# Kernel tuning notes

Measured on AMD Instinct MI355X. Metric: run time of the kernel, lower is better.

## Reference

```python
import jax, jax.numpy as jnp
import numpy as np

CTX_SIZE = 4096
LAYER = 1
N_EMBD = 1024
HEAD_SIZE = 64
B, T = 4, 4096


def setup_inputs() -> dict:
    key = jax.random.key(0)
    ks = jax.random.split(key, 4)
    s = 1.0 / np.sqrt(N_EMBD)
    return {
        "x": jax.random.normal(ks[0], (B, T, N_EMBD), dtype=jnp.float32),
        "Wq": jax.random.normal(ks[1], (N_EMBD, HEAD_SIZE), dtype=jnp.float32) * s,
        "bq": jnp.zeros((HEAD_SIZE,), dtype=jnp.float32),
        "Wk": jax.random.normal(ks[2], (N_EMBD, HEAD_SIZE), dtype=jnp.float32) * s,
        "bk": jnp.zeros((HEAD_SIZE,), dtype=jnp.float32),
        "Wv": jax.random.normal(ks[3], (N_EMBD, HEAD_SIZE), dtype=jnp.float32) * s,
        "bv": jnp.zeros((HEAD_SIZE,), dtype=jnp.float32),
    }


def reference(x, Wq, bq, Wk, bk, Wv, bv):
    Bx, Tx, C = x.shape
    t = CTX_SIZE // (2 ** LAYER)
    cut = min(Tx, t)  # static: shapes are concrete under jit

    k = x @ Wk + bk                      # [B, T, H]
    q = x[:, -cut:, :] @ Wq + bq         # [B, cut, H] (fade: queries on last cut tokens)
    v = x @ Wv + bv                      # [B, T, H]

    att = jnp.einsum("bqh,bkh->bqk", q, k) * (C ** -0.5)  # [B, cut, T]

    # row i corresponds to absolute query position (T - cut + i); causal: key j <= that pos
    q_pos = jnp.arange(cut) + (Tx - cut)   # [cut]
    k_pos = jnp.arange(Tx)                 # [T]
    mask = k_pos[None, :] <= q_pos[:, None]  # [cut, T], True = keep
    att = jnp.where(mask[None, :, :], att, -jnp.inf)
    att = jax.nn.softmax(att, axis=-1)
    # dropout p=0.0 (eval mode): identity

    out = jnp.einsum("bqk,bkh->bqh", att, v)  # [B, cut, H]
    return out
```

## Files before the change

kernel.cpp:

```cpp
#include <hip/hip_runtime.h>

#define BB 4
#define TT 4096
#define CUT 2048
#define CE 1024
#define HD 64
#define QSC 0.045084220027780106f

typedef unsigned short u16;
typedef unsigned int u32;
typedef __attribute__((ext_vector_type(8))) short bf16x8;
typedef __attribute__((ext_vector_type(4))) float f32x4;

__device__ __forceinline__ u16 f2b(float f) {
  union { float f; unsigned u; } v; v.f = f;
  unsigned r = v.u + 0x7fffu + ((v.u >> 16) & 1u);
  return (u16)(r >> 16);
}

__device__ __forceinline__ u32 cvtpk(float lo, float hi) {
  u32 r;
  asm("v_cvt_pk_bf16_f32 %0, %1, %2" : "=v"(r) : "v"(lo), "v"(hi));
  return r;
}

__device__ __forceinline__ void gld16(const u16* g, u16* l) {
  __builtin_amdgcn_global_load_lds((const __attribute__((address_space(1))) u32*)g,
                                   (__attribute__((address_space(3))) u32*)l, 16, 0, 0);
}

__global__ void wtrans_k(const float* __restrict__ Wk, const float* __restrict__ Wv,
                         const float* __restrict__ Wq, u16* __restrict__ w3f) {
  int id = blockIdx.x * 256 + threadIdx.x;
  int j    = id & 7;
  int lane = (id >> 3) & 63;
  int f    = id >> 9;
  int kstep = f & 31;
  int mnt   = f >> 5;
  int m  = mnt >> 2;
  int nt = mnt & 3;
  int k   = kstep * 32 + (lane >> 4) * 8 + j;
  int col = nt * 16 + (lane & 15);
  const float* W = (m == 0) ? Wk : (m == 1) ? Wv : Wq;
  w3f[id] = f2b(W[k * 64 + col]);
}

__launch_bounds__(256, 2)
__global__ void proj_k(const float* __restrict__ x, const u16* __restrict__ w3f,
                       const float* __restrict__ bk, const float* __restrict__ bv,
                       const float* __restrict__ bq,
                       u16* __restrict__ KF, u16* __restrict__ VF, u16* __restrict__ Qb) {
  __shared__ u16  st[2][2][12][512];
  __shared__ f32x4 cl[2][12][64];
  const int tid  = threadIdx.x;
  const int lane = tid & 63;
  const int wv   = tid >> 6;
  const int rg   = wv & 1;
  const int kh   = wv >> 1;
  const int l15  = lane & 15;
  const int g    = lane >> 4;
  const int r0   = blockIdx.x * 32;

  f32x4 acc[12];
  #pragma unroll
  for (int t = 0; t < 12; ++t) acc[t] = (f32x4){0.f, 0.f, 0.f, 0.f};

  const float* xrow = x + (size_t)(r0 + rg * 16 + l15) * CE + kh * 512;

  #define STAGE(buf, t)                                                        \
    {                                                                          \
      _Pragma("unroll")                                                        \
      for (int i = 0; i < 6; ++i) {                                            \
        int jj = wv * 6 + i;                                                   \
        int hh = jj / 12, mm = jj % 12;                                        \
        gld16(&w3f[(size_t)(mm * 32 + hh * 16 + (t)) * 512 + lane * 8],        \
              &st[buf][hh][mm][0]);                                            \
      }                                                                        \
    }

  f32x4 xs[2][2];
  STAGE(0, 0);
  __builtin_amdgcn_sched_barrier(0);
  xs[0][0] = *(const f32x4*)(xrow + g * 8);
  xs[0][1] = *(const f32x4*)(xrow + g * 8 + 4);
  asm volatile("s_waitcnt vmcnt(0)" ::: "memory");
  __builtin_amdgcn_s_barrier();

  #pragma unroll
  for (int t = 0; t < 16; ++t) {
    const int cur = t & 1, nxt = cur ^ 1;
    if (t < 15) {
      STAGE(nxt, t + 1);
      __builtin_amdgcn_sched_barrier(0);
      const float* xp = xrow + (t + 1) * 32 + g * 8;
      xs[nxt][0] = *(const f32x4*)xp;
      xs[nxt][1] = *(const f32x4*)(xp + 4);
      __builtin_amdgcn_sched_barrier(0);
    }
    bf16x8 a;
    #pragma unroll
    for (int j = 0; j < 4; ++j) {
      a[j]     = (short)f2b(xs[cur][0][j]);
      a[j + 4] = (short)f2b(xs[cur][1][j]);
    }
    #pragma unroll
    for (int mnt = 0; mnt < 12; ++mnt) {
      bf16x8 bfr = *(const bf16x8*)&st[cur][kh][mnt][lane * 8];
      acc[mnt] = __builtin_amdgcn_mfma_f32_16x16x32_bf16(a, bfr, acc[mnt], 0, 0, 0);
    }
    if (t < 15) {
      asm volatile("s_waitcnt vmcnt(2)" ::: "memory");
    } else {
      asm volatile("s_waitcnt vmcnt(0)" ::: "memory");
    }
    __builtin_amdgcn_s_barrier();
  }
  #undef STAGE

  if (kh == 1) {
    #pragma unroll
    for (int t = 0; t < 12; ++t) cl[rg][t][lane] = acc[t];
  }
  __syncthreads();
  if (kh == 0) {
    #pragma unroll
    for (int t = 0; t < 12; ++t) acc[t] += cl[rg][t][lane];

    const int b    = r0 >> 12;
    const int cch  = (r0 >> 6) & 63;
    const int half = (r0 >> 5) & 1;
    const int h    = rg;

    const int t0 = r0 & (TT - 1);
    if (t0 >= CUT) {
      const int trow = t0 - CUT + h * 16;
      #pragma unroll
      for (int nt = 0; nt < 4; ++nt) {
        int col = nt * 16 + l15;
        float bc = bq[col];
        #pragma unroll
        for (int r = 0; r < 4; ++r)
          Qb[((size_t)b * CUT + trow + g * 4 + r) * HD + col] =
              f2b((acc[8 + nt][r] + bc) * QSC);
      }
    }
    {
      u16* KFc = KF + ((size_t)(b * 64 + cch) * 8) * 512;
      const int kt2 = (half * 2 + h) * 2;
      #pragma unroll
      for (int nt = 0; nt < 4; ++nt) {
        int col = nt * 16 + l15;
        float bc = bk[col];
        f32x4 v = acc[nt];
        const int off = (kt2 + (nt >> 1)) * 512 + 128 * ((nt & 1) * 2 + (l15 >> 3)) + (l15 & 7);
        #pragma unroll
        for (int r = 0; r < 4; ++r)
          KFc[off + (g * 4 + r) * 8] = f2b(v[r] + bc);
      }
    }
    {
      u16* VFc = VF + ((size_t)(b * 64 + cch) * 8) * 512;
      #pragma unroll
      for (int nt = 0; nt < 4; ++nt) {
        int col = nt * 16 + l15;
        float bc = bv[col];
        f32x4 v = acc[4 + nt];
        #pragma unroll
        for (int r = 0; r < 4; ++r) {
          int tt = h * 16 + g * 4 + r;
          VFc[(half * 4 + nt) * 512 + (l15 + 16 * (tt >> 3)) * 8 + (tt & 7)] = f2b(v[r] + bc);
        }
      }
    }
  }
}

__launch_bounds__(512, 2)
__global__ void attn_k(const u16* __restrict__ Qb, const u16* __restrict__ KF,
                       const u16* __restrict__ VF, float* __restrict__ out) {
  __shared__ u32   PLd[8][16][36];
  __shared__ float OO[8][16][66];
  __shared__ float OL[8][32];
  const int tid  = threadIdx.x;
  const int lane = tid & 63;
  const int wv   = tid >> 6;
  const int l15  = lane & 15;
  const int g    = lane >> 4;
  const int id   = blockIdx.x;
  const int b    = id & 3;
  const int i0   = (id >> 2) * 32;

  const int qmin = CUT + i0;

  bf16x8 qf[2][2];
  #pragma unroll
  for (int h = 0; h < 2; ++h) {
    const u16* qrow = Qb + ((size_t)b * CUT + i0 + h * 16 + l15) * HD;
    qf[h][0] = *(const bf16x8*)&qrow[g * 8];
    qf[h][1] = *(const bf16x8*)&qrow[32 + g * 8];
  }

  f32x4 o[2][4];
  #pragma unroll
  for (int h = 0; h < 2; ++h)
    #pragma unroll
    for (int dt = 0; dt < 4; ++dt) o[h][dt] = (f32x4){0.f, 0.f, 0.f, 0.f};
  float lsum[2] = {0.f, 0.f};

  const int nch = (CUT + i0 + 32 + 63) >> 6;
  const u16* KFb = KF + (size_t)b * 64 * 8 * 512;
  const u16* VFb = VF + (size_t)b * 64 * 8 * 512;

  bf16x8 ka[4][2];
  {
    const u16* kp = KFb + (size_t)wv * 4096 + lane * 8;
    #pragma unroll
    for (int kt = 0; kt < 4; ++kt) {
      ka[kt][0] = *(const bf16x8*)(kp + (kt * 2 + 0) * 512);
      ka[kt][1] = *(const bf16x8*)(kp + (kt * 2 + 1) * 512);
    }
  }

  for (int c = wv; c < nch; c += 8) {
    const int kv0 = c << 6;

    const u16* vp = VFb + (size_t)c * 4096 + lane * 8;
    bf16x8 va[2][4];
    #pragma unroll
    for (int c2 = 0; c2 < 2; ++c2)
      #pragma unroll
      for (int dt = 0; dt < 4; ++dt)
        va[c2][dt] = *(const bf16x8*)(vp + (c2 * 4 + dt) * 512);

    bf16x8 kb[4][2];
    const int cn = c + 8;
    if (cn < nch) {
      const u16* kp = KFb + (size_t)cn * 4096 + lane * 8;
      #pragma unroll
      for (int kt = 0; kt < 4; ++kt) {
        kb[kt][0] = *(const bf16x8*)(kp + (kt * 2 + 0) * 512);
        kb[kt][1] = *(const bf16x8*)(kp + (kt * 2 + 1) * 512);
      }
    }

    f32x4 st[2][4];
    __builtin_amdgcn_s_setprio(1);
    #pragma unroll
    for (int h = 0; h < 2; ++h)
      #pragma unroll
      for (int kt = 0; kt < 4; ++kt) {
        f32x4 s = (f32x4){0.f, 0.f, 0.f, 0.f};
        s = __builtin_amdgcn_mfma_f32_16x16x32_bf16(ka[kt][0], qf[h][0], s, 0, 0, 0);
        s = __builtin_amdgcn_mfma_f32_16x16x32_bf16(ka[kt][1], qf[h][1], s, 0, 0, 0);
        st[h][kt] = s;
      }
    __builtin_amdgcn_s_setprio(0);

    #pragma unroll
    for (int h = 0; h < 2; ++h) {
      if (kv0 + 63 <= qmin + h * 16) {
        #pragma unroll
        for (int kt = 0; kt < 4; ++kt)
          #pragma unroll
          for (int r = 0; r < 4; ++r) {
            float p = exp2f(st[h][kt][r]);
            st[h][kt][r] = p;
            lsum[h] += p;
          }
      } else {
        const int qabs = qmin + h * 16 + l15;
        #pragma unroll
        for (int kt = 0; kt < 4; ++kt)
          #pragma unroll
          for (int r = 0; r < 4; ++r) {
            int key = kv0 + kt * 16 + g * 4 + r;
            float p = exp2f(st[h][kt][r]);
            p = (key <= qabs) ? p : 0.f;
            st[h][kt][r] = p;
            lsum[h] += p;
          }
      }
    }

    #pragma unroll
    for (int h = 0; h < 2; ++h) {
      #pragma unroll
      for (int kt = 0; kt < 4; ++kt) {
        u32 d0 = cvtpk(st[h][kt][0], st[h][kt][1]);
        u32 d1 = cvtpk(st[h][kt][2], st[h][kt][3]);
        u32* p = &PLd[wv][l15][kt * 8 + g * 2];
        p[0] = d0; p[1] = d1;
      }
      __builtin_amdgcn_s_setprio(1);
      #pragma unroll
      for (int c2 = 0; c2 < 2; ++c2) {
        bf16x8 pa = *(const bf16x8*)&PLd[wv][l15][c2 * 16 + g * 4];
        #pragma unroll
        for (int dt = 0; dt < 4; ++dt)
          o[h][dt] = __builtin_amdgcn_mfma_f32_16x16x32_bf16(pa, va[c2][dt], o[h][dt], 0, 0, 0);
      }
      __builtin_amdgcn_s_setprio(0);
    }

    if (cn < nch) {
      #pragma unroll
      for (int kt = 0; kt < 4; ++kt) {
        ka[kt][0] = kb[kt][0];
        ka[kt][1] = kb[kt][1];
      }
    }
  }

  #pragma unroll
  for (int h = 0; h < 2; ++h) {
    float ls = lsum[h];
    ls += __shfl_xor(ls, 16);
    ls += __shfl_xor(ls, 32);
    if (lane < 16) OL[wv][h * 16 + l15] = ls;
  }

  #pragma unroll
  for (int ph = 0; ph < 2; ++ph) {
    #pragma unroll
    for (int dt = 0; dt < 4; ++dt)
      #pragma unroll
      for (int r = 0; r < 4; ++r)
        OO[wv][g * 4 + r][dt * 16 + l15] = o[ph][dt][r];
    __syncthreads();
    #pragma unroll
    for (int e = tid; e < 1024; e += 512) {
      int q = e >> 6, d = e & 63;
      float L = 0.f, O = 0.f;
      #pragma unroll
      for (int w = 0; w < 8; ++w) { L += OL[w][ph * 16 + q]; O += OO[w][q][d]; }
      out[((size_t)b * CUT + i0 + ph * 16 + q) * HD + d] = O / L;
    }
    __syncthreads();
  }
}

extern "C" void kernel_launch(void* const* d_in, const int* in_sizes, int n_in,
                              void* d_out, int out_size, void* d_ws, size_t ws_size,
                              hipStream_t stream) {
  const float* x  = (const float*)d_in[0];
  const float* Wq = (const float*)d_in[1];
  const float* bq = (const float*)d_in[2];
  const float* Wk = (const float*)d_in[3];
  const float* bk = (const float*)d_in[4];
  const float* Wv = (const float*)d_in[5];
  const float* bv = (const float*)d_in[6];
  float* out = (float*)d_out;

  u16* Qb  = (u16*)d_ws;
  u16* W3F = Qb + (size_t)BB * CUT * HD;
  u16* KF  = W3F + (size_t)384 * 512;
  u16* VF  = KF + (size_t)BB * 64 * 8 * 512;

  wtrans_k<<<768, 256, 0, stream>>>(Wk, Wv, Wq, W3F);
  proj_k<<<512, 256, 0, stream>>>(x, W3F, bk, bv, bq, KF, VF, Qb);
  attn_k<<<256, 512, 0, stream>>>(Qb, KF, VF, out);
}
```

Before: 47.72 us.

## Split projection output tiles across twice as many waves in proj_k

Doubles the proj_k block from 256 to 512 threads. Each wave now computes 6 of the 12 output column tiles instead of all 12, and the weight staging loads and epilogue writes (K, V, Q) are divided between the two new halves. The aim is more waves in flight to hide the latency of the x loads and the MFMA chains, with fewer accumulator registers per wave. In exchange, every wave still loads and converts the same x fragment, so global reads of x are duplicated, and the split-K reduction buffer is reshaped to match.

New measurement: 52.52 us. 1.1x slower.

```diff
diff --git a/kernel.cpp b/kernel.cpp
--- a/kernel.cpp
+++ b/kernel.cpp
@@ -45,33 +45,34 @@
   w3f[id] = f2b(W[k * 64 + col]);
 }
 
-__launch_bounds__(256, 2)
+__launch_bounds__(512, 4)
 __global__ void proj_k(const float* __restrict__ x, const u16* __restrict__ w3f,
                        const float* __restrict__ bk, const float* __restrict__ bv,
                        const float* __restrict__ bq,
                        u16* __restrict__ KF, u16* __restrict__ VF, u16* __restrict__ Qb) {
   __shared__ u16  st[2][2][12][512];
-  __shared__ f32x4 cl[2][12][64];
+  __shared__ f32x4 cl[2][2][6][64];
   const int tid  = threadIdx.x;
   const int lane = tid & 63;
   const int wv   = tid >> 6;
   const int rg   = wv & 1;
-  const int kh   = wv >> 1;
+  const int kh   = (wv >> 1) & 1;
+  const int nh   = wv >> 2;
   const int l15  = lane & 15;
   const int g    = lane >> 4;
   const int r0   = blockIdx.x * 32;
 
-  f32x4 acc[12];
-  #pragma unroll
-  for (int t = 0; t < 12; ++t) acc[t] = (f32x4){0.f, 0.f, 0.f, 0.f};
+  f32x4 acc[6];
+  #pragma unroll
+  for (int t = 0; t < 6; ++t) acc[t] = (f32x4){0.f, 0.f, 0.f, 0.f};
 
   const float* xrow = x + (size_t)(r0 + rg * 16 + l15) * CE + kh * 512;
 
   #define STAGE(buf, t)                                                        \
     {                                                                          \
       _Pragma("unroll")                                                        \
-      for (int i = 0; i < 6; ++i) {                                            \
-        int jj = wv * 6 + i;                                                   \
+      for (int i = 0; i < 3; ++i) {                                            \
+        int jj = wv * 3 + i;                                                   \
         int hh = jj / 12, mm = jj % 12;                                        \
         gld16(&w3f[(size_t)(mm * 32 + hh * 16 + (t)) * 512 + lane * 8],        \
               &st[buf][hh][mm][0]);                                            \
@@ -104,9 +105,9 @@
       a[j + 4] = (short)f2b(xs[cur][1][j]);
     }
     #pragma unroll
-    for (int mnt = 0; mnt < 12; ++mnt) {
-      bf16x8 bfr = *(const bf16x8*)&st[cur][kh][mnt][lane * 8];
-      acc[mnt] = __builtin_amdgcn_mfma_f32_16x16x32_bf16(a, bfr, acc[mnt], 0, 0, 0);
+    for (int j = 0; j < 6; ++j) {
+      bf16x8 bfr = *(const bf16x8*)&st[cur][kh][nh * 6 + j][lane * 8];
+      acc[j] = __builtin_amdgcn_mfma_f32_16x16x32_bf16(a, bfr, acc[j], 0, 0, 0);
     }
     if (t < 15) {
       asm volatile("s_waitcnt vmcnt(2)" ::: "memory");
@@ -119,32 +120,19 @@
 
   if (kh == 1) {
     #pragma unroll
-    for (int t = 0; t < 12; ++t) cl[rg][t][lane] = acc[t];
+    for (int t = 0; t < 6; ++t) cl[rg][nh][t][lane] = acc[t];
   }
   __syncthreads();
   if (kh == 0) {
     #pragma unroll
-    for (int t = 0; t < 12; ++t) acc[t] += cl[rg][t][lane];
+    for (int t = 0; t < 6; ++t) acc[t] += cl[rg][nh][t][lane];
 
     const int b    = r0 >> 12;
     const int cch  = (r0 >> 6) & 63;
     const int half = (r0 >> 5) & 1;
     const int h    = rg;
 
-    const int t0 = r0 & (TT - 1);
-    if (t0 >= CUT) {
-      const int trow = t0 - CUT + h * 16;
-      #pragma unroll
-      for (int nt = 0; nt < 4; ++nt) {
-        int col = nt * 16 + l15;
-        float bc = bq[col];
-        #pragma unroll
-        for (int r = 0; r < 4; ++r)
-          Qb[((size_t)b * CUT + trow + g * 4 + r) * HD + col] =
-              f2b((acc[8 + nt][r] + bc) * QSC);
-      }
-    }
-    {
+    if (nh == 0) {
       u16* KFc = KF + ((size_t)(b * 64 + cch) * 8) * 512;
       const int kt2 = (half * 2 + h) * 2;
       #pragma unroll
@@ -157,11 +145,9 @@
         for (int r = 0; r < 4; ++r)
           KFc[off + (g * 4 + r) * 8] = f2b(v[r] + bc);
       }
-    }
-    {
       u16* VFc = VF + ((size_t)(b * 64 + cch) * 8) * 512;
       #pragma unroll
-      for (int nt = 0; nt < 4; ++nt) {
+      for (int nt = 0; nt < 2; ++nt) {
         int col = nt * 16 + l15;
         float bc = bv[col];
         f32x4 v = acc[4 + nt];
@@ -169,6 +155,33 @@
         for (int r = 0; r < 4; ++r) {
           int tt = h * 16 + g * 4 + r;
           VFc[(half * 4 + nt) * 512 + (l15 + 16 * (tt >> 3)) * 8 + (tt & 7)] = f2b(v[r] + bc);
+        }
+      }
+    } else {
+      u16* VFc = VF + ((size_t)(b * 64 + cch) * 8) * 512;
+      #pragma unroll
+      for (int nt = 2; nt < 4; ++nt) {
+        int col = nt * 16 + l15;
+        float bc = bv[col];
+        f32x4 v = acc[nt - 2];
+        #pragma unroll
+        for (int r = 0; r < 4; ++r) {
+          int tt = h * 16 + g * 4 + r;
+          VFc[(half * 4 + nt) * 512 + (l15 + 16 * (tt >> 3)) * 8 + (tt & 7)] = f2b(v[r] + bc);
+        }
+      }
+      const int t0 = r0 & (TT - 1);
+      if (t0 >= CUT) {
+        const int trow = t0 - CUT + h * 16;
+        #pragma unroll
+        for (int nt = 0; nt < 4; ++nt) {
+          int col = nt * 16 + l15;
+          float bc = bq[col];
+          f32x4 v = acc[2 + nt];
+          #pragma unroll
+          for (int r = 0; r < 4; ++r)
+            Qb[((size_t)b * CUT + trow + g * 4 + r) * HD + col] =
+                f2b((v[r] + bc) * QSC);
         }
       }
     }
@@ -357,6 +370,6 @@
   u16* VF  = KF + (size_t)BB * 64 * 8 * 512;
 
   wtrans_k<<<768, 256, 0, stream>>>(Wk, Wv, Wq, W3F);
-  proj_k<<<512, 256, 0, stream>>>(x, W3F, bk, bv, bq, KF, VF, Qb);
+  proj_k<<<512, 512, 0, stream>>>(x, W3F, bk, bv, bq, KF, VF, Qb);
   attn_k<<<256, 512, 0, stream>>>(Qb, KF, VF, out);
 }
```

## Give each projection wave a full K range over 64 rows, dropping split-K reduction

Applied to the files above, without the earlier changes.

The projection kernel now processes 64 rows per block, with each of the four waves owning 16 rows across the whole 1024-wide reduction, instead of splitting K across wave pairs. This removes the LDS partial-sum exchange and the extra barrier, and each staged weight tile is reused by four row groups instead of two. Grid size halves to 256 blocks and the occupancy hint rises to 3. The trade-off is fewer blocks to fill the GPU, more in-flight x loads per wave, and larger per-stage weight staging.

Measured after the change: 48.96 us. 2.6% more time.

```diff
diff --git a/kernel.cpp b/kernel.cpp
--- a/kernel.cpp
+++ b/kernel.cpp
@@ -45,45 +45,46 @@
   w3f[id] = f2b(W[k * 64 + col]);
 }
 
-__launch_bounds__(256, 2)
+__launch_bounds__(256, 3)
 __global__ void proj_k(const float* __restrict__ x, const u16* __restrict__ w3f,
                        const float* __restrict__ bk, const float* __restrict__ bv,
                        const float* __restrict__ bq,
                        u16* __restrict__ KF, u16* __restrict__ VF, u16* __restrict__ Qb) {
-  __shared__ u16  st[2][2][12][512];
-  __shared__ f32x4 cl[2][12][64];
+  __shared__ u16 st[2][12][1024];
   const int tid  = threadIdx.x;
   const int lane = tid & 63;
   const int wv   = tid >> 6;
-  const int rg   = wv & 1;
-  const int kh   = wv >> 1;
   const int l15  = lane & 15;
   const int g    = lane >> 4;
-  const int r0   = blockIdx.x * 32;
+  const int r0   = blockIdx.x * 64;
 
   f32x4 acc[12];
   #pragma unroll
   for (int t = 0; t < 12; ++t) acc[t] = (f32x4){0.f, 0.f, 0.f, 0.f};
 
-  const float* xrow = x + (size_t)(r0 + rg * 16 + l15) * CE + kh * 512;
+  const float* xrow = x + (size_t)(r0 + wv * 16 + l15) * CE;
 
   #define STAGE(buf, t)                                                        \
     {                                                                          \
       _Pragma("unroll")                                                        \
       for (int i = 0; i < 6; ++i) {                                            \
         int jj = wv * 6 + i;                                                   \
-        int hh = jj / 12, mm = jj % 12;                                        \
-        gld16(&w3f[(size_t)(mm * 32 + hh * 16 + (t)) * 512 + lane * 8],        \
-              &st[buf][hh][mm][0]);                                            \
+        int mm = jj >> 1, hk = jj & 1;                                         \
+        gld16(&w3f[(size_t)(mm * 32 + 2 * (t) + hk) * 512 + lane * 8],         \
+              &st[buf][mm][hk * 512]);                                         \
       }                                                                        \
     }
 
-  f32x4 xs[2][2];
+  f32x4 xs[2][2][2];
   STAGE(0, 0);
   __builtin_amdgcn_sched_barrier(0);
-  xs[0][0] = *(const f32x4*)(xrow + g * 8);
-  xs[0][1] = *(const f32x4*)(xrow + g * 8 + 4);
-  asm volatile("s_waitcnt vmcnt(0)" ::: "memory");
+  #pragma unroll
+  for (int kc = 0; kc < 2; ++kc) {
+    const float* xp = xrow + kc * 32 + g * 8;
+    xs[0][kc][0] = *(const f32x4*)xp;
+    xs[0][kc][1] = *(const f32x4*)(xp + 4);
+  }
+  asm volatile("s_waitcnt vmcnt(4)" ::: "memory");
   __builtin_amdgcn_s_barrier();
 
   #pragma unroll
@@ -92,84 +93,81 @@
     if (t < 15) {
       STAGE(nxt, t + 1);
       __builtin_amdgcn_sched_barrier(0);
-      const float* xp = xrow + (t + 1) * 32 + g * 8;
-      xs[nxt][0] = *(const f32x4*)xp;
-      xs[nxt][1] = *(const f32x4*)(xp + 4);
+      #pragma unroll
+      for (int kc = 0; kc < 2; ++kc) {
+        const float* xp = xrow + (t + 1) * 64 + kc * 32 + g * 8;
+        xs[nxt][kc][0] = *(const f32x4*)xp;
+        xs[nxt][kc][1] = *(const f32x4*)(xp + 4);
+      }
       __builtin_amdgcn_sched_barrier(0);
     }
-    bf16x8 a;
-    #pragma unroll
-    for (int j = 0; j < 4; ++j) {
-      a[j]     = (short)f2b(xs[cur][0][j]);
-      a[j + 4] = (short)f2b(xs[cur][1][j]);
-    }
-    #pragma unroll
-    for (int mnt = 0; mnt < 12; ++mnt) {
-      bf16x8 bfr = *(const bf16x8*)&st[cur][kh][mnt][lane * 8];
-      acc[mnt] = __builtin_amdgcn_mfma_f32_16x16x32_bf16(a, bfr, acc[mnt], 0, 0, 0);
+    #pragma unroll
+    for (int kc = 0; kc < 2; ++kc) {
+      bf16x8 a;
+      #pragma unroll
+      for (int j = 0; j < 4; ++j) {
+        a[j]     = (short)f2b(xs[cur][kc][0][j]);
+        a[j + 4] = (short)f2b(xs[cur][kc][1][j]);
+      }
+      #pragma unroll
+      for (int mnt = 0; mnt < 12; ++mnt) {
+        bf16x8 bfr = *(const bf16x8*)&st[cur][mnt][kc * 512 + lane * 8];
+        acc[mnt] = __builtin_amdgcn_mfma_f32_16x16x32_bf16(a, bfr, acc[mnt], 0, 0, 0);
+      }
     }
     if (t < 15) {
-      asm volatile("s_waitcnt vmcnt(2)" ::: "memory");
-    } else {
-      asm volatile("s_waitcnt vmcnt(0)" ::: "memory");
-    }
-    __builtin_amdgcn_s_barrier();
+      asm volatile("s_waitcnt vmcnt(4)" ::: "memory");
+      __builtin_amdgcn_s_barrier();
+    }
   }
   #undef STAGE
 
-  if (kh == 1) {
-    #pragma unroll
-    for (int t = 0; t < 12; ++t) cl[rg][t][lane] = acc[t];
-  }
-  __syncthreads();
-  if (kh == 0) {
-    #pragma unroll
-    for (int t = 0; t < 12; ++t) acc[t] += cl[rg][t][lane];
-
-    const int b    = r0 >> 12;
-    const int cch  = (r0 >> 6) & 63;
-    const int half = (r0 >> 5) & 1;
-    const int h    = rg;
-
+  const int b    = r0 >> 12;
+  const int cch  = (r0 >> 6) & 63;
+  const int half = wv >> 1;
+  const int h    = wv & 1;
+
+  {
+    u16* KFc = KF + ((size_t)(b * 64 + cch) * 8) * 512;
+    const int kt2 = (half * 2 + h) * 2;
+    #pragma unroll
+    for (int nt = 0; nt < 4; ++nt) {
+      int col = nt * 16 + l15;
+      float bc = bk[col];
+      f32x4 v = acc[nt];
+      const int off = (kt2 + (nt >> 1)) * 512 + 128 * ((nt & 1) * 2 + (l15 >> 3)) + (l15 & 7);
+      #pragma unroll
+      for (int r = 0; r < 4; ++r)
+        KFc[off + (g * 4 + r) * 8] = f2b(v[r] + bc);
+    }
+  }
+  {
+    u16* VFc = VF + ((size_t)(b * 64 + cch) * 8) * 512;
+    #pragma unroll
+    for (int nt = 0; nt < 4; ++nt) {
+      int col = nt * 16 + l15;
+      float bc = bv[col];
+      f32x4 v = acc[4 + nt];
+      #pragma unroll
+      for (int r = 0; r < 4; ++r) {
+        int tt = h * 16 + g * 4 + r;
+        VFc[(half * 4 + nt) * 512 + (l15 + 16 * (tt >> 3)) * 8 + (tt & 7)] = f2b(v[r] + bc);
+      }
+    }
+  }
+  {
     const int t0 = r0 & (TT - 1);
     if (t0 >= CUT) {
-      const int trow = t0 - CUT + h * 16;
+      const int trow = t0 - CUT + wv * 16;
       #pragma unroll
       for (int nt = 0; nt < 4; ++nt) {
         int col = nt * 16 + l15;
         float bc = bq[col];
+        f32x4 v = acc[8 + nt];
         #pragma unroll
         for (int r = 0; r < 4; ++r)
           Qb[((size_t)b * CUT + trow + g * 4 + r) * HD + col] =
-              f2b((acc[8 + nt][r] + bc) * QSC);
-      }
-    }
-    {
-      u16* KFc = KF + ((size_t)(b * 64 + cch) * 8) * 512;
-      const int kt2 = (half * 2 + h) * 2;
-      #pragma unroll
-      for (int nt = 0; nt < 4; ++nt) {
-        int col = nt * 16 + l15;
-        float bc = bk[col];
-        f32x4 v = acc[nt];
-        const int off = (kt2 + (nt >> 1)) * 512 + 128 * ((nt & 1) * 2 + (l15 >> 3)) + (l15 & 7);
-        #pragma unroll
-        for (int r = 0; r < 4; ++r)
-          KFc[off + (g * 4 + r) * 8] = f2b(v[r] + bc);
-      }
-    }
-    {
-      u16* VFc = VF + ((size_t)(b * 64 + cch) * 8) * 512;
-      #pragma unroll
-      for (int nt = 0; nt < 4; ++nt) {
-        int col = nt * 16 + l15;
-        float bc = bv[col];
-        f32x4 v = acc[4 + nt];
-        #pragma unroll
-        for (int r = 0; r < 4; ++r) {
-          int tt = h * 16 + g * 4 + r;
-          VFc[(half * 4 + nt) * 512 + (l15 + 16 * (tt >> 3)) * 8 + (tt & 7)] = f2b(v[r] + bc);
-        }
+              f2b((v[r] + bc) * QSC);
       }
     }
   }
@@ -357,6 +355,6 @@
   u16* VF  = KF + (size_t)BB * 64 * 8 * 512;
 
   wtrans_k<<<768, 256, 0, stream>>>(Wk, Wv, Wq, W3F);
-  proj_k<<<512, 256, 0, stream>>>(x, W3F, bk, bv, bq, KF, VF, Qb);
+  proj_k<<<256, 256, 0, stream>>>(x, W3F, bk, bv, bq, KF, VF, Qb);
   attn_k<<<256, 512, 0, stream>>>(Qb, KF, VF, out);
 }
```
